# Kernel optimization log

Measured on AMD Instinct MI355X. Metric: run time of the kernel, lower is better.

The kernel has to match this reference:

```python
import jax, jax.numpy as jnp
import numpy as np

NUM_GROUPS = 32
NUM_HEADS = 8
EPS = 1e-5


def group_norm(x, gamma, beta):
    B, C, H, W = x.shape
    g = NUM_GROUPS
    xg = x.reshape(B, g, C // g, H, W)
    mean = xg.mean(axis=(2, 3, 4), keepdims=True)
    var = xg.var(axis=(2, 3, 4), keepdims=True)
    xn = ((xg - mean) * jax.lax.rsqrt(var + EPS)).reshape(B, C, H, W)
    return xn * gamma[None, :, None, None] + beta[None, :, None, None]


def setup_inputs() -> dict:
    key = jax.random.key(0)
    ks = jax.random.split(key, 7)
    B, C, H, W = 16, 512, 32, 32
    x = jax.random.normal(ks[0], (B, C, H, W), dtype=jnp.float32)
    norm_w = jnp.ones((C,), jnp.float32)
    norm_b = jnp.zeros((C,), jnp.float32)
    s1 = 1.0 / np.sqrt(C)
    qkv_w = jax.random.uniform(ks[1], (3 * C, C), jnp.float32, -s1, s1)
    qkv_b = jax.random.uniform(ks[2], (3 * C,), jnp.float32, -s1, s1)
    proj_w = jax.random.uniform(ks[3], (C, C), jnp.float32, -s1, s1)
    proj_b = jax.random.uniform(ks[4], (C,), jnp.float32, -s1, s1)
    return {"x": x, "norm_w": norm_w, "norm_b": norm_b,
            "qkv_w": qkv_w, "qkv_b": qkv_b,
            "proj_w": proj_w, "proj_b": proj_b}


def reference(x, norm_w, norm_b, qkv_w, qkv_b, proj_w, proj_b):
    B, C, H, W = x.shape
    nh = NUM_HEADS
    hd = C // nh
    S = H * W
    h = group_norm(x, norm_w, norm_b)
    # 1x1 conv == channel matmul: [B,3C,H,W]
    qkv = jnp.einsum('oc,bchw->bohw', qkv_w, h) + qkv_b[None, :, None, None]
    q, k, v = jnp.split(qkv, 3, axis=1)
    # q,v -> [B, nh, S, hd]; k -> [B, nh, hd, S]
    q = q.reshape(B, nh, hd, S).transpose(0, 1, 3, 2)
    k = k.reshape(B, nh, hd, S)
    v = v.reshape(B, nh, hd, S).transpose(0, 1, 3, 2)
    scale = 1.0 / np.sqrt(hd)
    attn = jnp.einsum('bhsd,bhdt->bhst', q, k) * scale
    attn = jax.nn.softmax(attn, axis=-1)
    out = jnp.einsum('bhst,bhtd->bhsd', attn, v)  # [B,nh,S,hd]
    out = out.transpose(0, 1, 3, 2).reshape(B, C, H, W)
    out = jnp.einsum('oc,bchw->bohw', proj_w, out) + proj_b[None, :, None, None]
    return out + x
```

## Files before the change

kernel.cpp:

```cpp
#include <hip/hip_runtime.h>
#include <hip/hip_bf16.h>
#include <stdint.h>

#define B_N 16
#define C_N 512
#define S_N 1024
#define G_N 32
#define NH  8
#define HD  64

typedef __attribute__((ext_vector_type(8))) short bf16x8;
typedef __attribute__((ext_vector_type(4))) float f32x4;
typedef __attribute__((ext_vector_type(16))) float f32x16;
typedef unsigned short u16;
typedef unsigned int   u32;
typedef __attribute__((ext_vector_type(4))) u16 u16x4;
typedef __attribute__((ext_vector_type(4))) u32 u32x4;

#define SC2F 0.18033688011112042f

__device__ __forceinline__ u16 f2bf(float f) {
  u32 u = __builtin_bit_cast(u32, f);
  u32 r = (u + 0x7fffu + ((u >> 16) & 1u)) >> 16;
  return (u16)r;
}

__device__ __forceinline__ u32 cvtpk(float a, float b) {
  u32 r;
  asm("v_cvt_pk_bf16_f32 %0, %1, %2" : "=v"(r) : "v"(a), "v"(b));
  return r;
}

__device__ __forceinline__ void gll16(const void* g, void* l) {
  __builtin_amdgcn_global_load_lds((const __attribute__((address_space(1))) u32*)g,
                                   (__attribute__((address_space(3))) u32*)l, 16, 0, 0);
}

__global__ __launch_bounds__(256) void gn_stats(const float* __restrict__ x,
                                                float* __restrict__ stats) {
  const int bg = blockIdx.x;
  const float4* xv = (const float4*)(x + (size_t)bg * (16 * S_N));
  float s = 0.f, ss = 0.f;
  for (int i = threadIdx.x; i < 4096; i += 256) {
    float4 v = xv[i];
    s  += v.x + v.y + v.z + v.w;
    ss += v.x*v.x + v.y*v.y + v.z*v.z + v.w*v.w;
  }
  #pragma unroll
  for (int m = 1; m < 64; m <<= 1) { s += __shfl_xor(s, m); ss += __shfl_xor(ss, m); }
  __shared__ float red[2][4];
  const int wid = threadIdx.x >> 6;
  if ((threadIdx.x & 63) == 0) { red[0][wid] = s; red[1][wid] = ss; }
  __syncthreads();
  if (threadIdx.x == 0) {
    float S1 = red[0][0]+red[0][1]+red[0][2]+red[0][3];
    float S2 = red[1][0]+red[1][1]+red[1][2]+red[1][3];
    float mean = S1 * (1.f/16384.f);
    float var  = S2 * (1.f/16384.f) - mean*mean;
    stats[bg*2]   = mean;
    stats[bg*2+1] = rsqrtf(var + 1e-5f);
  }
}

__global__ __launch_bounds__(256) void gn_apply_t(const float* __restrict__ x,
                                                  const float* __restrict__ stats,
                                                  const float* __restrict__ nw,
                                                  const float* __restrict__ nb,
                                                  u16* __restrict__ h_t) {
  const int c0 = blockIdx.x * 32, s0 = blockIdx.y * 64, b = blockIdx.z;
  __shared__ u16 tile[32][68];
  const int t = threadIdx.x;
  #pragma unroll
  for (int i = 0; i < 2; i++) {
    int idx4 = (i*256 + t) * 4;
    int cr = idx4 >> 6, sr = idx4 & 63;
    int c = c0 + cr;
    float4 v = *(const float4*)&x[((size_t)b*C_N + c)*S_N + s0 + sr];
    int bg = b*G_N + (c >> 4);
    float mean = stats[bg*2], rstd = stats[bg*2+1];
    float w = nw[c]*rstd;
    float bb = nb[c] - mean*w;
    tile[cr][sr]   = f2bf(v.x*w + bb);
    tile[cr][sr+1] = f2bf(v.y*w + bb);
    tile[cr][sr+2] = f2bf(v.z*w + bb);
    tile[cr][sr+3] = f2bf(v.w*w + bb);
  }
  __syncthreads();
  #pragma unroll
  for (int i = 0; i < 2; i++) {
    int idx = i*256 + t;
    int sr = idx >> 3;
    int cr4 = (idx & 7) * 4;
    u16x4 v = { tile[cr4][sr], tile[cr4+1][sr], tile[cr4+2][sr], tile[cr4+3][sr] };
    *(u16x4*)&h_t[((size_t)b*S_N + s0 + sr)*C_N + c0 + cr4] = v;
  }
}

__global__ __launch_bounds__(256) void cvt_bf16_all(const float* __restrict__ qkvw,
                                                    const float* __restrict__ projw,
                                                    u16* __restrict__ qw,
                                                    u16* __restrict__ pw) {
  int i = blockIdx.x*256 + threadIdx.x;
  const float4* src; u16x4* dst; int j;
  if (i < 196608) { src = (const float4*)qkvw; dst = (u16x4*)qw; j = i; }
  else            { src = (const float4*)projw; dst = (u16x4*)pw; j = i - 196608; }
  float4 v = src[j];
  u16x4 r = { f2bf(v.x), f2bf(v.y), f2bf(v.z), f2bf(v.w) };
  dst[j] = r;
}

__global__ __launch_bounds__(256) void gemm_qkv(const u16* __restrict__ h_t,
                                                const u16* __restrict__ wq,
                                                const float* __restrict__ bq,
                                                u16* __restrict__ Qp,
                                                u16* __restrict__ Kp,
                                                u16* __restrict__ Vp) {
  __shared__ u16 Ash[128*32];
  __shared__ u16 Bsh[128*32];
  const int n0 = blockIdx.x*128, m0 = blockIdx.y*128, b = blockIdx.z;
  const int tid = threadIdx.x, wid = tid >> 6, lane = tid & 63;
  const int wm = wid >> 1, wn = wid & 1;
  const u16* Ag = h_t + (size_t)b*S_N*C_N;
  const f32x4 vzero = {0.f,0.f,0.f,0.f};
  f32x4 acc[4][4];
  #pragma unroll
  for (int i=0;i<4;i++)
    #pragma unroll
    for (int j=0;j<4;j++) acc[i][j] = vzero;

  const int arow = lane >> 2, aslot = (lane & 3) * 8;
  for (int k0 = 0; k0 < C_N; k0 += 32) {
    __syncthreads();
    #pragma unroll
    for (int i = 0; i < 2; i++) {
      int r = wid*32 + i*16 + arow;
      gll16(Ag + (size_t)(m0+r)*C_N + k0 + aslot, &Ash[(wid*32+i*16)*32]);
      gll16(wq + (size_t)(n0+r)*C_N + k0 + aslot, &Bsh[(wid*32+i*16)*32]);
    }
    __syncthreads();
    bf16x8 aF[4], bF[4];
    #pragma unroll
    for (int mi=0;mi<4;mi++)
      aF[mi] = *(const bf16x8*)&Ash[(wm*64+mi*16+(lane&15))*32 + (lane>>4)*8];
    #pragma unroll
    for (int ni=0;ni<4;ni++)
      bF[ni] = *(const bf16x8*)&Bsh[(wn*64+ni*16+(lane&15))*32 + (lane>>4)*8];
    #pragma unroll
    for (int mi=0;mi<4;mi++)
      #pragma unroll
      for (int ni=0;ni<4;ni++)
        acc[mi][ni] = __builtin_amdgcn_mfma_f32_16x16x32_bf16(aF[mi], bF[ni], acc[mi][ni], 0, 0, 0);
  }

  #pragma unroll
  for (int mi=0;mi<4;mi++) {
    #pragma unroll
    for (int ni=0;ni<4;ni++) {
      int o = n0 + wn*64 + ni*16 + (lane & 15);
      float bias = bq[o];
      int sec = o >> 9;
      int oo  = o & 511;
      int hh  = oo >> 6, d = oo & 63;
      size_t bh = (size_t)(b*NH + hh);
      float qsc = (sec == 0) ? SC2F : 1.0f;
      #pragma unroll
      for (int r=0;r<4;r++) {
        int s = m0 + wm*64 + mi*16 + (lane>>4)*4 + r;
        u16 bv = f2bf((acc[mi][ni][r] + bias) * qsc);
        if (sec == 0)      Qp[(bh*S_N + s)*HD + d] = bv;
        else if (sec == 1) Kp[(bh*S_N + s)*HD + d] = bv;
        else               Vp[(bh*HD + d)*S_N + s] = bv;
      }
    }
  }
}

__device__ __forceinline__ void attn_tile_body(const u16* __restrict__ Kb,
                                               const u16* __restrict__ Vb,
                                               u16* __restrict__ KlC, u16* __restrict__ VlC,
                                               u16* __restrict__ KlN, u16* __restrict__ VlN,
                                               const bf16x8 (&qf)[4], const bf16x8 onesf,
                                               f32x16 (&oacc)[2], f32x16& oacc_l,
                                               int it, int l31, int hi,
                                               int ra, int rb, int ca, int cb, int wid) {
  const int t0 = it * 64;
  asm volatile("s_waitcnt vmcnt(0)" ::: "memory");
  __syncthreads();

  if (it < 15) {
    const int tn = t0 + 64;
    gll16(Kb + (size_t)(tn + ra)*HD + ca, &KlN[(wid*16    )*64]);
    gll16(Kb + (size_t)(tn + rb)*HD + cb, &KlN[(wid*16 + 8)*64]);
    gll16(Vb + (size_t)ra*S_N + tn + ca,  &VlN[(wid*16    )*64]);
    gll16(Vb + (size_t)rb*S_N + tn + cb,  &VlN[(wid*16 + 8)*64]);
  }

  bf16x8 kF[2][4];
  #pragma unroll
  for (int tt=0;tt<2;tt++)
    #pragma unroll
    for (int kt=0;kt<4;kt++) {
      int row = tt*32 + l31;
      int phys = (kt*2 + hi) ^ (row & 7);
      kF[tt][kt] = *(const bf16x8*)&KlC[row*64 + phys*8];
    }

  f32x16 st[2];
  #pragma unroll
  for (int tt=0;tt<2;tt++)
    #pragma unroll
    for (int i=0;i<16;i++) st[tt][i] = 0.f;
  __builtin_amdgcn_s_setprio(1);
  #pragma unroll
  for (int tt=0;tt<2;tt++)
    #pragma unroll
    for (int kt=0;kt<4;kt++)
      st[tt] = __builtin_amdgcn_mfma_f32_32x32x16_bf16(kF[tt][kt], qf[kt], st[tt], 0, 0, 0);
  __builtin_amdgcn_s_setprio(0);

  #pragma unroll
  for (int tt=0;tt<2;tt++)
    #pragma unroll
    for (int i=0;i<16;i++)
      st[tt][i] = exp2f(st[tt][i]);

  u32x4 paw[4];
  #pragma unroll
  for (int ks=0;ks<4;ks++) {
    float p0 = st[ks>>1][(ks&1)*8+0], p1 = st[ks>>1][(ks&1)*8+1];
    float p2 = st[ks>>1][(ks&1)*8+2], p3 = st[ks>>1][(ks&1)*8+3];
    float p4 = st[ks>>1][(ks&1)*8+4], p5 = st[ks>>1][(ks&1)*8+5];
    float p6 = st[ks>>1][(ks&1)*8+6], p7 = st[ks>>1][(ks&1)*8+7];
    u32 w0 = cvtpk(p0, p1);
    u32 w1 = cvtpk(p2, p3);
    u32 w2 = cvtpk(p4, p5);
    u32 w3 = cvtpk(p6, p7);
    u32 s0 = hi ? w0 : w2;
    u32 s1 = hi ? w1 : w3;
    u32 r0 = (u32)__shfl_xor((int)s0, 32);
    u32 r1 = (u32)__shfl_xor((int)s1, 32);
    u32x4 w = { hi ? r0 : w0, hi ? r1 : w1, hi ? w2 : r0, hi ? w3 : r1 };
    paw[ks] = w;
  }

  __builtin_amdgcn_s_setprio(1);
  #pragma unroll
  for (int ks=0;ks<4;ks++) {
    bf16x8 pb = __builtin_bit_cast(bf16x8, paw[ks]);
    oacc_l = __builtin_amdgcn_mfma_f32_32x32x16_bf16(onesf, pb, oacc_l, 0, 0, 0);
    #pragma unroll
    for (int dt=0;dt<2;dt++) {
      int row = dt*32 + l31;
      int phys = (ks*2 + hi) ^ (row & 7);
      bf16x8 vF = *(const bf16x8*)&VlC[row*64 + phys*8];
      oacc[dt] = __builtin_amdgcn_mfma_f32_32x32x16_bf16(vF, pb, oacc[dt], 0, 0, 0);
    }
  }
  __builtin_amdgcn_s_setprio(0);

  __syncthreads();
}

__global__ __launch_bounds__(256) void attn_fwd(const u16* __restrict__ Qp,
                                                const u16* __restrict__ Kp,
                                                const u16* __restrict__ Vp,
                                                u16* __restrict__ at) {
  __shared__ u16 Kl[2][64*64];
  __shared__ u16 Vl[2][64*64];
  const int hh = blockIdx.x, q0 = blockIdx.y*128, b = blockIdx.z;
  const int tid = threadIdx.x, wid = tid >> 6, lane = tid & 63;
  const int l31 = lane & 31, hi = lane >> 5;
  const size_t bh = (size_t)(b*NH + hh);
  const u16* Qb = Qp + bh*(S_N*HD);
  const u16* Kb = Kp + bh*(S_N*HD);
  const u16* Vb = Vp + bh*(HD*S_N);
  const int s = q0 + wid*32 + l31;

  bf16x8 qf[4];
  #pragma unroll
  for (int kt=0;kt<4;kt++)
    qf[kt] = *(const bf16x8*)&Qb[(size_t)s*HD + kt*16 + hi*8];

  const u32x4 onesw = {0x3F803F80u, 0x3F803F80u, 0x3F803F80u, 0x3F803F80u};
  const bf16x8 onesf = __builtin_bit_cast(bf16x8, onesw);

  f32x16 oacc[2], oacc_l;
  #pragma unroll
  for (int dt=0;dt<2;dt++)
    #pragma unroll
    for (int i=0;i<16;i++) oacc[dt][i] = 0.f;
  #pragma unroll
  for (int i=0;i<16;i++) oacc_l[i] = 0.f;

  const int ra = wid*16 + (lane >> 3);
  const int rb = ra + 8;
  const int ca = (((lane & 7) ^ (ra & 7)) * 8);
  const int cb = (((lane & 7) ^ (rb & 7)) * 8);

  gll16(Kb + (size_t)ra*HD + ca,  &Kl[0][(wid*16    )*64]);
  gll16(Kb + (size_t)rb*HD + cb,  &Kl[0][(wid*16 + 8)*64]);
  gll16(Vb + (size_t)ra*S_N + ca, &Vl[0][(wid*16    )*64]);
  gll16(Vb + (size_t)rb*S_N + cb, &Vl[0][(wid*16 + 8)*64]);

  #pragma unroll 1
  for (int it = 0; it < 16; it += 2) {
    attn_tile_body(Kb, Vb, Kl[0], Vl[0], Kl[1], Vl[1], qf, onesf, oacc, oacc_l,
                   it,     l31, hi, ra, rb, ca, cb, wid);
    attn_tile_body(Kb, Vb, Kl[1], Vl[1], Kl[0], Vl[0], qf, onesf, oacc, oacc_l,
                   it + 1, l31, hi, ra, rb, ca, cb, wid);
  }

  float inv = 1.0f / oacc_l[0];
  #pragma unroll
  for (int dt=0;dt<2;dt++)
    #pragma unroll
    for (int qd=0;qd<4;qd++) {
      int dbase = 4*hi + 8*qd + 32*dt;
      u16x4 o;
      #pragma unroll
      for (int j=0;j<4;j++) o[j] = f2bf(oacc[dt][qd*4+j] * inv);
      *(u16x4*)&at[((size_t)b*S_N + s)*C_N + hh*HD + dbase] = o;
    }
}

__global__ __launch_bounds__(256) void gemm_proj(const u16* __restrict__ pwb,
                                                 const u16* __restrict__ at,
                                                 const float* __restrict__ bp,
                                                 const float* __restrict__ x,
                                                 float* __restrict__ out) {
  __shared__ u16 Ash[128*32];
  __shared__ u16 Bsh[128*32];
  const int n0 = blockIdx.x*128, m0 = blockIdx.y*128, b = blockIdx.z;
  const int tid = threadIdx.x, wid = tid >> 6, lane = tid & 63;
  const int wm = wid >> 1, wn = wid & 1;
  const u16* Bg = at + (size_t)b*S_N*C_N;
  const f32x4 vzero = {0.f,0.f,0.f,0.f};
  f32x4 acc[4][4];
  #pragma unroll
  for (int i=0;i<4;i++)
    #pragma unroll
    for (int j=0;j<4;j++) acc[i][j] = vzero;

  const int arow = lane >> 2, aslot = (lane & 3) * 8;
  for (int k0 = 0; k0 < C_N; k0 += 32) {
    __syncthreads();
    #pragma unroll
    for (int i = 0; i < 2; i++) {
      int r = wid*32 + i*16 + arow;
      gll16(pwb + (size_t)(m0+r)*C_N + k0 + aslot, &Ash[(wid*32+i*16)*32]);
      gll16(Bg  + (size_t)(n0+r)*C_N + k0 + aslot, &Bsh[(wid*32+i*16)*32]);
    }
    __syncthreads();
    bf16x8 aF[4], bF[4];
    #pragma unroll
    for (int mi=0;mi<4;mi++)
      aF[mi] = *(const bf16x8*)&Ash[(wm*64+mi*16+(lane&15))*32 + (lane>>4)*8];
    #pragma unroll
    for (int ni=0;ni<4;ni++)
      bF[ni] = *(const bf16x8*)&Bsh[(wn*64+ni*16+(lane&15))*32 + (lane>>4)*8];
    #pragma unroll
    for (int mi=0;mi<4;mi++)
      #pragma unroll
      for (int ni=0;ni<4;ni++)
        acc[mi][ni] = __builtin_amdgcn_mfma_f32_16x16x32_bf16(aF[mi], bF[ni], acc[mi][ni], 0, 0, 0);
  }

  #pragma unroll
  for (int mi=0;mi<4;mi++) {
    #pragma unroll
    for (int ni=0;ni<4;ni++) {
      int ss = n0 + wn*64 + ni*16 + (lane & 15);
      #pragma unroll
      for (int r=0;r<4;r++) {
        int o = m0 + wm*64 + mi*16 + (lane>>4)*4 + r;
        size_t idx = ((size_t)b*C_N + o)*S_N + ss;
        out[idx] = acc[mi][ni][r] + bp[o] + x[idx];
      }
    }
  }
}

extern "C" void kernel_launch(void* const* d_in, const int* in_sizes, int n_in,
                              void* d_out, int out_size, void* d_ws, size_t ws_size,
                              hipStream_t stream) {
  const float* x     = (const float*)d_in[0];
  const float* nw    = (const float*)d_in[1];
  const float* nb    = (const float*)d_in[2];
  const float* qkvw  = (const float*)d_in[3];
  const float* qkvb  = (const float*)d_in[4];
  const float* projw = (const float*)d_in[5];
  const float* projb = (const float*)d_in[6];
  float* out = (float*)d_out;

  char* ws = (char*)d_ws;
  float* stats = (float*)ws;
  u16* h_t = (u16*)(ws + 4096);
  u16* qw  = (u16*)(ws + 4096 + 16777216);
  u16* pw  = (u16*)((char*)qw + 1572864);
  u16* Qp  = (u16*)((char*)pw + 524288);
  u16* Kp  = (u16*)((char*)Qp + 16777216);
  u16* Vp  = (u16*)((char*)Kp + 16777216);
  u16* at  = (u16*)((char*)Vp + 16777216);

  gn_stats    <<<512, 256, 0, stream>>>(x, stats);
  gn_apply_t  <<<dim3(16,16,16), 256, 0, stream>>>(x, stats, nw, nb, h_t);
  cvt_bf16_all<<<1024, 256, 0, stream>>>(qkvw, projw, qw, pw);
  gemm_qkv    <<<dim3(12,8,16), 256, 0, stream>>>(h_t, qw, qkvb, Qp, Kp, Vp);
  attn_fwd    <<<dim3(8,8,16), 256, 0, stream>>>(Qp, Kp, Vp, at);
  gemm_proj   <<<dim3(8,4,16), 256, 0, stream>>>(pw, at, projb, x, out);
}
```

Before: 256.3 us.

## Double-buffer LDS tiles in QKV and projection GEMMs to overlap loads

Both GEMM kernels now use two shared-memory buffers per operand. The next K-slice is issued via direct global-to-LDS loads while MFMAs run on the current slice, which hides global load latency that was previously exposed between the two barriers. LDS usage per block doubles, which may reduce occupancy. A trailing __syncthreads at the end of an attention helper is also removed.

```diff
diff --git a/kernel.cpp b/kernel.cpp
--- a/kernel.cpp
+++ b/kernel.cpp
@@ -115,8 +115,8 @@
                                                 u16* __restrict__ Qp,
                                                 u16* __restrict__ Kp,
                                                 u16* __restrict__ Vp) {
-  __shared__ u16 Ash[128*32];
-  __shared__ u16 Bsh[128*32];
+  __shared__ u16 Ash[2][128*32];
+  __shared__ u16 Bsh[2][128*32];
   const int n0 = blockIdx.x*128, m0 = blockIdx.y*128, b = blockIdx.z;
   const int tid = threadIdx.x, wid = tid >> 6, lane = tid & 63;
   const int wm = wid >> 1, wn = wid & 1;
@@ -129,27 +129,41 @@
     for (int j=0;j<4;j++) acc[i][j] = vzero;
 
   const int arow = lane >> 2, aslot = (lane & 3) * 8;
-  for (int k0 = 0; k0 < C_N; k0 += 32) {
-    __syncthreads();
+
+  auto stage = [&](u16* Adst, u16* Bdst, int k0s) {
     #pragma unroll
     for (int i = 0; i < 2; i++) {
       int r = wid*32 + i*16 + arow;
-      gll16(Ag + (size_t)(m0+r)*C_N + k0 + aslot, &Ash[(wid*32+i*16)*32]);
-      gll16(wq + (size_t)(n0+r)*C_N + k0 + aslot, &Bsh[(wid*32+i*16)*32]);
-    }
-    __syncthreads();
+      gll16(Ag + (size_t)(m0+r)*C_N + k0s + aslot, &Adst[(wid*32+i*16)*32]);
+      gll16(wq + (size_t)(n0+r)*C_N + k0s + aslot, &Bdst[(wid*32+i*16)*32]);
+    }
+  };
+  auto compute = [&](const u16* AshC, const u16* BshC) {
     bf16x8 aF[4], bF[4];
     #pragma unroll
     for (int mi=0;mi<4;mi++)
-      aF[mi] = *(const bf16x8*)&Ash[(wm*64+mi*16+(lane&15))*32 + (lane>>4)*8];
+      aF[mi] = *(const bf16x8*)&AshC[(wm*64+mi*16+(lane&15))*32 + (lane>>4)*8];
     #pragma unroll
     for (int ni=0;ni<4;ni++)
-      bF[ni] = *(const bf16x8*)&Bsh[(wn*64+ni*16+(lane&15))*32 + (lane>>4)*8];
+      bF[ni] = *(const bf16x8*)&BshC[(wn*64+ni*16+(lane&15))*32 + (lane>>4)*8];
     #pragma unroll
     for (int mi=0;mi<4;mi++)
       #pragma unroll
       for (int ni=0;ni<4;ni++)
         acc[mi][ni] = __builtin_amdgcn_mfma_f32_16x16x32_bf16(aF[mi], bF[ni], acc[mi][ni], 0, 0, 0);
+  };
+
+  stage(Ash[0], Bsh[0], 0);
+  #pragma unroll 1
+  for (int k0 = 0; k0 < C_N; k0 += 64) {
+    asm volatile("s_waitcnt vmcnt(0)" ::: "memory");
+    __syncthreads();
+    stage(Ash[1], Bsh[1], k0 + 32);
+    compute(Ash[0], Bsh[0]);
+    asm volatile("s_waitcnt vmcnt(0)" ::: "memory");
+    __syncthreads();
+    if (k0 + 64 < C_N) stage(Ash[0], Bsh[0], k0 + 64);
+    compute(Ash[1], Bsh[1]);
   }
 
   #pragma unroll
@@ -257,8 +271,6 @@
     }
   }
   __builtin_amdgcn_s_setprio(0);
-
-  __syncthreads();
 }
 
 __global__ __launch_bounds__(256) void attn_fwd(const u16* __restrict__ Qp,
@@ -328,8 +340,8 @@
                                                  const float* __restrict__ bp,
                                                  const float* __restrict__ x,
                                                  float* __restrict__ out) {
-  __shared__ u16 Ash[128*32];
-  __shared__ u16 Bsh[128*32];
+  __shared__ u16 Ash[2][128*32];
+  __shared__ u16 Bsh[2][128*32];
   const int n0 = blockIdx.x*128, m0 = blockIdx.y*128, b = blockIdx.z;
   const int tid = threadIdx.x, wid = tid >> 6, lane = tid & 63;
   const int wm = wid >> 1, wn = wid & 1;
@@ -342,27 +354,41 @@
     for (int j=0;j<4;j++) acc[i][j] = vzero;
 
   const int arow = lane >> 2, aslot = (lane & 3) * 8;
-  for (int k0 = 0; k0 < C_N; k0 += 32) {
-    __syncthreads();
+
+  auto stage = [&](u16* Adst, u16* Bdst, int k0s) {
     #pragma unroll
     for (int i = 0; i < 2; i++) {
       int r = wid*32 + i*16 + arow;
-      gll16(pwb + (size_t)(m0+r)*C_N + k0 + aslot, &Ash[(wid*32+i*16)*32]);
-      gll16(Bg  + (size_t)(n0+r)*C_N + k0 + aslot, &Bsh[(wid*32+i*16)*32]);
-    }
-    __syncthreads();
+      gll16(pwb + (size_t)(m0+r)*C_N + k0s + aslot, &Adst[(wid*32+i*16)*32]);
+      gll16(Bg  + (size_t)(n0+r)*C_N + k0s + aslot, &Bdst[(wid*32+i*16)*32]);
+    }
+  };
+  auto compute = [&](const u16* AshC, const u16* BshC) {
     bf16x8 aF[4], bF[4];
     #pragma unroll
     for (int mi=0;mi<4;mi++)
-      aF[mi] = *(const bf16x8*)&Ash[(wm*64+mi*16+(lane&15))*32 + (lane>>4)*8];
+      aF[mi] = *(const bf16x8*)&AshC[(wm*64+mi*16+(lane&15))*32 + (lane>>4)*8];
     #pragma unroll
     for (int ni=0;ni<4;ni++)
-      bF[ni] = *(const bf16x8*)&Bsh[(wn*64+ni*16+(lane&15))*32 + (lane>>4)*8];
+      bF[ni] = *(const bf16x8*)&BshC[(wn*64+ni*16+(lane&15))*32 + (lane>>4)*8];
     #pragma unroll
     for (int mi=0;mi<4;mi++)
       #pragma unroll
       for (int ni=0;ni<4;ni++)
         acc[mi][ni] = __builtin_amdgcn_mfma_f32_16x16x32_bf16(aF[mi], bF[ni], acc[mi][ni], 0, 0, 0);
+  };
+
+  stage(Ash[0], Bsh[0], 0);
+  #pragma unroll 1
+  for (int k0 = 0; k0 < C_N; k0 += 64) {
+    asm volatile("s_waitcnt vmcnt(0)" ::: "memory");
+    __syncthreads();
+    stage(Ash[1], Bsh[1], k0 + 32);
+    compute(Ash[0], Bsh[0]);
+    asm volatile("s_waitcnt vmcnt(0)" ::: "memory");
+    __syncthreads();
+    if (k0 + 64 < C_N) stage(Ash[0], Bsh[0], k0 + 64);
+    compute(Ash[1], Bsh[1]);
   }
 
   #pragma unroll
```

Measured after the change: 259.6 us. About the same (+1.3%).
